# Kernel tuning notes

Hardware: AMD Instinct MI355X
Metric: run time of the kernel (lower is better)

Reference implementation:

```python
import jax, jax.numpy as jnp
import numpy as np


def setup_inputs() -> dict:
    key = jax.random.key(0)
    ks = jax.random.split(key, 32)
    B, S, H, E, Vs, T = 32, 400, 512, 300, 200, 32
    EN, V = 50000, 50200
    rn = lambda k, shape, s=0.05: jax.random.normal(k, shape, jnp.float32) * s
    return {
        'encoder_hidden': rn(ks[0], (B, S, 2 * H), 1.0),
        'hidden0': rn(ks[1], (B, H), 1.0),
        'user_embed': rn(ks[2], (B, E), 1.0),
        'W_embed': rn(ks[3], (EN, E), 1.0),
        'W_ih': rn(ks[4], (3 * H, E)), 'W_hh': rn(ks[5], (3 * H, H)),
        'b_ih': rn(ks[6], (3 * H,)), 'b_hh': rn(ks[7], (3 * H,)),
        'Wk_c': rn(ks[8], (2 * H, H)), 'bk_c': rn(ks[9], (H,)),
        'Wq_c': rn(ks[10], (H, H)), 'bq_c': rn(ks[11], (H,)),
        'we_c': rn(ks[12], (H,)), 'be_c': rn(ks[13], (1,)),
        'Wk_u': rn(ks[14], (E, H)), 'bk_u': rn(ks[15], (H,)),
        'Wq_u': rn(ks[16], (H, H)), 'bq_u': rn(ks[17], (H,)),
        'we_u': rn(ks[18], (H,)), 'be_u': rn(ks[19], (1,)),
        'Wc': rn(ks[20], (3 * H + 2 * E, H)),
        'Wg': rn(ks[21], (3 * H + E,)), 'bg': rn(ks[22], (1,)),
        'Wgen': rn(ks[23], (H, EN)),
        'src_mask': jnp.ones((B, S), jnp.int32),
        'tgt_': jax.random.randint(ks[24], (B, T), 0, EN),
        'specific_vocab': jax.random.randint(ks[25], (B, Vs), 0, EN),
        'vocab_size': V,
    }


def reference(encoder_hidden, hidden0, user_embed, W_embed, W_ih, W_hh, b_ih, b_hh,
              Wk_c, bk_c, Wq_c, bq_c, we_c, be_c, Wk_u, bk_u, Wq_u, bq_u, we_u, be_u,
              Wc, Wg, bg, Wgen, src_mask, tgt_, specific_vocab, vocab_size):
    B, T = tgt_.shape
    # teacher forcing: prev token embed, step 0 uses <s> token id 1
    tgt_embed = W_embed[tgt_]                                  # [B,T,E]
    init_embed = jnp.broadcast_to(W_embed[1], (B, 1, W_embed.shape[1]))
    prev = jnp.concatenate([init_embed, tgt_embed[:, :T - 1]], axis=1)
    xs = jnp.swapaxes(prev, 0, 1)                              # [T,B,E]

    user_vocab_emb = W_embed[specific_vocab]                   # [B,Vs,E]
    proj_key_c = encoder_hidden @ Wk_c + bk_c                  # [B,S,H]
    proj_key_u = user_vocab_emb @ Wk_u + bk_u                  # [B,Vs,H]
    mask = src_mask != 0
    batch_idx = jnp.arange(B)[:, None]

    def gru_cell(h, x):
        gi = x @ W_ih.T + b_ih
        gh = h @ W_hh.T + b_hh
        i_r, i_z, i_n = jnp.split(gi, 3, axis=-1)
        h_r, h_z, h_n = jnp.split(gh, 3, axis=-1)
        r = jax.nn.sigmoid(i_r + h_r)
        z = jax.nn.sigmoid(i_z + h_z)
        n = jnp.tanh(i_n + r * h_n)
        return (1.0 - z) * n + z * h

    def step(h, x):
        h = gru_cell(h, x)                                     # [B,H]
        q = h
        # Bahdanau attention over encoder states
        sc = jnp.tanh((q @ Wq_c + bq_c)[:, None, :] + proj_key_c) @ we_c + be_c  # [B,S]
        sc = jnp.where(mask, sc, -1e9)
        ac = jax.nn.softmax(sc, axis=-1)
        ctx_c = jnp.einsum('bs,bsd->bd', ac, encoder_hidden)   # [B,2H]
        # Bahdanau attention over user-specific vocab embeddings
        su = jnp.tanh((q @ Wq_u + bq_u)[:, None, :] + proj_key_u) @ we_u + be_u  # [B,Vs]
        au = jax.nn.softmax(su, axis=-1)
        ctx_u = jnp.einsum('bv,bve->be', au, user_vocab_emb)   # [B,E]
        ch = jnp.tanh(jnp.concatenate([q, ctx_c, ctx_u, user_embed], axis=-1) @ Wc)
        gen_prob = jax.nn.softmax(ch @ Wgen, axis=-1)          # [B,embed_num]
        gen_prob = jnp.pad(gen_prob, ((0, 0), (0, vocab_size - gen_prob.shape[-1])))
        copy_prob = jnp.zeros((B, vocab_size), gen_prob.dtype).at[batch_idx, specific_vocab].add(au)
        copy_p = jax.nn.sigmoid(jnp.concatenate([ctx_c, q, ctx_u], axis=-1) @ Wg + bg[0])[:, None]
        mix = copy_p * copy_prob + (1.0 - copy_p) * gen_prob   # [B,vocab]
        return h, mix

    _, probs = jax.lax.scan(step, hidden0, xs)                 # [T,B,V]
    return jnp.swapaxes(probs, 0, 1)                           # [B,T,V]
```

## Files before the change

### kernel.cpp

```cpp
#include <hip/hip_runtime.h>


typedef __attribute__((ext_vector_type(8))) short short8;
typedef __attribute__((ext_vector_type(4))) float f32x4;
typedef unsigned short us;

__device__ __forceinline__ float bf2f(us u) {
  return __uint_as_float(((unsigned)u) << 16);
}
__device__ __forceinline__ us f2bf(float f) {
  unsigned x = __float_as_uint(f);
  unsigned r = x + 0x7fffu + ((x >> 16) & 1u);
  return (us)(r >> 16);
}
__device__ __forceinline__ float fsigmoid(float x) { return 1.f / (1.f + __expf(-x)); }
__device__ __forceinline__ float ftanh(float x) {
  float t = __expf(-2.f * fabsf(x));
  float r = (1.f - t) / (1.f + t);
  return x >= 0.f ? r : -r;
}
__device__ __forceinline__ float ftanh_fast(float x) {
  float u = exp2f(-2.8853900817779268f * fabsf(x));
  float r = (1.f - u) * __builtin_amdgcn_rcpf(1.f + u);
  return copysignf(r, x);
}


__global__ __launch_bounds__(256) void k_cast_f2b(const float* __restrict__ src,
                                                  us* __restrict__ dst, int n4) {
  int stride = gridDim.x * blockDim.x;
  for (int i = blockIdx.x * blockDim.x + threadIdx.x; i < n4; i += stride) {
    float4 v = ((const float4*)src)[i];
    ushort4 o;
    o.x = f2bf(v.x); o.y = f2bf(v.y); o.z = f2bf(v.z); o.w = f2bf(v.w);
    ((ushort4*)dst)[i] = o;
  }
}

__global__ __launch_bounds__(256) void k_tcastX(const float* __restrict__ src0,
                                                us* __restrict__ dst0,
                                                int R, int C, int Rpad,
                                                size_t srcB, size_t dstB) {
  __shared__ float tile[32][33];
  const float* src = src0 + (size_t)blockIdx.z * srcB;
  us* dst = dst0 + (size_t)blockIdx.z * dstB;
  int c0 = blockIdx.x * 32, r0 = blockIdx.y * 32;
  int tx = threadIdx.x & 31, ty = threadIdx.x >> 5;
#pragma unroll
  for (int i = 0; i < 4; ++i) {
    int r = r0 + ty + i * 8, c = c0 + tx;
    tile[ty + i * 8][tx] = (r < R && c < C) ? src[(size_t)r * C + c] : 0.f;
  }
  __syncthreads();
#pragma unroll
  for (int i = 0; i < 4; ++i) {
    int c = c0 + ty + i * 8, rr = r0 + tx;
    if (c < C && rr < Rpad) dst[(size_t)c * Rpad + rr] = f2bf(tile[tx][ty + i * 8]);
  }
}

__global__ __launch_bounds__(256) void k_tcastXb(const us* __restrict__ src0,
                                                 us* __restrict__ dst0,
                                                 int R, int C, int Rpad,
                                                 size_t srcB, size_t dstB) {
  __shared__ us tile[32][33];
  const us* src = src0 + (size_t)blockIdx.z * srcB;
  us* dst = dst0 + (size_t)blockIdx.z * dstB;
  int c0 = blockIdx.x * 32, r0 = blockIdx.y * 32;
  int tx = threadIdx.x & 31, ty = threadIdx.x >> 5;
#pragma unroll
  for (int i = 0; i < 4; ++i) {
    int r = r0 + ty + i * 8, c = c0 + tx;
    tile[ty + i * 8][tx] = (r < R && c < C) ? src[(size_t)r * C + c] : (us)0;
  }
  __syncthreads();
#pragma unroll
  for (int i = 0; i < 4; ++i) {
    int c = c0 + ty + i * 8, rr = r0 + tx;
    if (c < C && rr < Rpad) dst[(size_t)c * Rpad + rr] = tile[tx][ty + i * 8];
  }
}

__global__ __launch_bounds__(64) void k_castpad(const float* __restrict__ src,
                                                us* __restrict__ dst,
                                                int C, int Cpad) {
  int row = blockIdx.x;
  for (int k = threadIdx.x; k < Cpad; k += 64)
    dst[(size_t)row * Cpad + k] = (k < C) ? f2bf(src[(size_t)row * C + k]) : (us)0;
}

__global__ __launch_bounds__(64) void k_gather_xe(const float* __restrict__ W_embed,
                                                  const int* __restrict__ tgt,
                                                  us* __restrict__ xe) {
  int r = blockIdx.x;
  int t = r >> 5, b = r & 31;
  int tok = (t == 0) ? 1 : tgt[b * 32 + (t - 1)];
  const float* src = W_embed + (size_t)tok * 300;
  for (int k = threadIdx.x; k < 320; k += 64)
    xe[(size_t)r * 320 + k] = (k < 300) ? f2bf(src[k]) : (us)0;
}

__global__ __launch_bounds__(64) void k_gather_uve(const float* __restrict__ W_embed,
                                                   const int* __restrict__ sv,
                                                   us* __restrict__ uve) {
  int row = blockIdx.x;
  int tok = sv[row];
  const float* src = W_embed + (size_t)tok * 300;
  for (int k = threadIdx.x; k < 320; k += 64)
    uve[(size_t)row * 320 + k] = (k < 300) ? f2bf(src[k]) : (us)0;
}

__global__ __launch_bounds__(64) void k_fragpack(const float* __restrict__ W,
                                                 us* __restrict__ F) {
  int q = blockIdx.x, lt = blockIdx.y, kt = blockIdx.z, l = threadIdx.x;
  int localrow = lt * 16 + (l & 15);
  int g = localrow >> 6, jj = localrow & 63;
  const float* src = W + (size_t)(g * 512 + q * 64 + jj) * 512 + kt * 32 + (l >> 4) * 8;
  us* dst = F + (((size_t)(q * 12 + lt) * 16 + kt) * 64 + l) * 8;
#pragma unroll
  for (int i = 0; i < 8; ++i) dst[i] = f2bf(src[i]);
}

template <int MODE>
__global__ __launch_bounds__(512) void gemm_bt(const us* __restrict__ A,
                                               const us* __restrict__ BT,
                                               int M, int N, int K, int Ntiles,
                                               const float* __restrict__ bias,
                                               us* __restrict__ outB,
                                               float* __restrict__ outF,
                                               float* __restrict__ rowsum) {
  __shared__ us As[256 * 32];
  __shared__ us Bs[128 * 32];
  __shared__ float rs[256];
  const int tid = threadIdx.x;
  const int lane = tid & 63, wid = tid >> 6;
  const int wr = wid >> 1, wc = wid & 1;
  const int bx = blockIdx.x;
  const int mt = bx / Ntiles, nt = bx - mt * Ntiles;
  const int m0 = mt * 256, n0 = nt * 128;
  f32x4 acc[4][4] = {};
  for (int kk = 0; kk < K; kk += 32) {
    uint4 av0, av1, bv;
    {
      int c = tid, row = c >> 2, c8 = (c & 3) * 8;
      av0 = *(const uint4*)(A + (size_t)(m0 + row) * K + kk + c8);
      c = tid + 512; row = c >> 2; c8 = (c & 3) * 8;
      av1 = *(const uint4*)(A + (size_t)(m0 + row) * K + kk + c8);
      c = tid; row = c >> 2; c8 = (c & 3) * 8;
      int nr = n0 + row; if (nr > N - 1) nr = N - 1;
      bv = *(const uint4*)(BT + (size_t)nr * K + kk + c8);
    }
    __syncthreads();
    ((uint4*)As)[tid] = av0;
    ((uint4*)As)[tid + 512] = av1;
    ((uint4*)Bs)[tid] = bv;
    __syncthreads();
    short8 af[4], bfr[4];
#pragma unroll
    for (int m = 0; m < 4; ++m)
      af[m] = *(const short8*)(As + (wr * 64 + m * 16 + (lane & 15)) * 32 + (lane >> 4) * 8);
#pragma unroll
    for (int n = 0; n < 4; ++n)
      bfr[n] = *(const short8*)(Bs + (wc * 64 + n * 16 + (lane & 15)) * 32 + (lane >> 4) * 8);
#pragma unroll
    for (int m = 0; m < 4; ++m)
#pragma unroll
      for (int n = 0; n < 4; ++n)
        acc[m][n] = __builtin_amdgcn_mfma_f32_16x16x32_bf16(af[m], bfr[n], acc[m][n], 0, 0, 0);
  }
  if (MODE == 0) {
#pragma unroll
    for (int m = 0; m < 4; ++m)
#pragma unroll
      for (int n = 0; n < 4; ++n)
#pragma unroll
        for (int reg = 0; reg < 4; ++reg) {
          int r = m0 + wr * 64 + m * 16 + (lane >> 4) * 4 + reg;
          int c = n0 + wc * 64 + n * 16 + (lane & 15);
          outB[(size_t)r * N + c] = f2bf(acc[m][n][reg] + bias[c]);
        }
  } else {
    if (tid < 256) rs[tid] = 0.f;
    __syncthreads();
#pragma unroll
    for (int m = 0; m < 4; ++m) {
#pragma unroll
      for (int reg = 0; reg < 4; ++reg) {
        int rloc = wr * 64 + m * 16 + (lane >> 4) * 4 + reg;
        int r = m0 + rloc;
        size_t obase = (size_t)((r & 31) * 32 + (r >> 5)) * 50200;
        float s = 0.f;
#pragma unroll
        for (int n = 0; n < 4; ++n) {
          int c = n0 + wc * 64 + n * 16 + (lane & 15);
          if (c < N) {
            float e = __expf(acc[m][n][reg]);
            if (MODE == 1) outF[obase + c] = e;
            else outB[obase + c] = f2bf(e);
            s += e;
          }
        }
        s += __shfl_xor(s, 1, 64); s += __shfl_xor(s, 2, 64);
        s += __shfl_xor(s, 4, 64); s += __shfl_xor(s, 8, 64);
        if ((lane & 15) == 0) atomicAdd(&rs[rloc], s);
      }
    }
    __syncthreads();
    if (tid < 256) atomicAdd(&rowsum[m0 + tid], rs[tid]);
  }
}

template <int MODE>
__global__ __launch_bounds__(256) void gemm_med(const us* __restrict__ A,
                                                const us* __restrict__ BT,
                                                int M, int N, int K, int Ntiles,
                                                const float* __restrict__ bias,
                                                us* __restrict__ outB) {
  __shared__ us As[64 * 32];
  __shared__ us Bs[128 * 32];
  const int tid = threadIdx.x, lane = tid & 63, w = tid >> 6;
  const int bx = blockIdx.x;
  const int mt = bx / Ntiles, nt = bx - mt * Ntiles;
  const int m0 = mt * 64, n0 = nt * 128;
  f32x4 acc[4][2] = {};
  for (int kk = 0; kk < K; kk += 32) {
    uint4 av, bv0, bv1;
    av = *(const uint4*)(A + (size_t)(m0 + (tid >> 2)) * K + kk + (tid & 3) * 8);
    {
      int i0 = tid * 2, i1 = tid * 2 + 1;
      bv0 = *(const uint4*)(BT + (size_t)(n0 + (i0 >> 2)) * K + kk + (i0 & 3) * 8);
      bv1 = *(const uint4*)(BT + (size_t)(n0 + (i1 >> 2)) * K + kk + (i1 & 3) * 8);
    }
    __syncthreads();
    ((uint4*)As)[tid] = av;
    ((uint4*)Bs)[tid * 2] = bv0;
    ((uint4*)Bs)[tid * 2 + 1] = bv1;
    __syncthreads();
    short8 af[4], bf0, bf1;
#pragma unroll
    for (int m = 0; m < 4; ++m)
      af[m] = *(const short8*)(As + (m * 16 + (lane & 15)) * 32 + (lane >> 4) * 8);
    bf0 = *(const short8*)(Bs + ((w * 2 + 0) * 16 + (lane & 15)) * 32 + (lane >> 4) * 8);
    bf1 = *(const short8*)(Bs + ((w * 2 + 1) * 16 + (lane & 15)) * 32 + (lane >> 4) * 8);
#pragma unroll
    for (int m = 0; m < 4; ++m) {
      acc[m][0] = __builtin_amdgcn_mfma_f32_16x16x32_bf16(af[m], bf0, acc[m][0], 0, 0, 0);
      acc[m][1] = __builtin_amdgcn_mfma_f32_16x16x32_bf16(af[m], bf1, acc[m][1], 0, 0, 0);
    }
  }
#pragma unroll
  for (int m = 0; m < 4; ++m)
#pragma unroll
    for (int q = 0; q < 2; ++q)
#pragma unroll
      for (int reg = 0; reg < 4; ++reg) {
        int r = m0 + m * 16 + (lane >> 4) * 4 + reg;
        int c = n0 + (w * 2 + q) * 16 + (lane & 15);
        float v = acc[m][q][reg];
        if (MODE == 0) v += bias[c];
        else v = ftanh_fast(v);
        outB[(size_t)r * N + c] = f2bf(v);
      }
}

struct FP {
  const us* frag; const us* gib; const float* bhh; const float* hidden0;
  us* hball; float* hfall; int* arrive;
  const us* encb; const us* WkcT; const float* bkc; us* pkc;
  const us* uve; const us* WkuT; const float* bku; us* pku;
  const float* Wgen; us* WT;
  const float* enc; us* encTp;
  us* uveTp;
};

__device__ void gru_body(const FP& P, int q, int tid, char* pool) {
  us* hs = (us*)pool;
  float* gh = (float*)(pool + 32768);
  const int lane = tid & 63, w = tid >> 6;
  short8 bfr[16];
  {
    const us* fb = P.frag + (((size_t)(q * 12 + w) * 16) * 64 + lane) * 8;
#pragma unroll
    for (int kt = 0; kt < 16; ++kt) bfr[kt] = *(const short8*)(fb + (size_t)kt * 512);
  }
  float hprev[3];
#pragma unroll
  for (int s = 0; s < 3; ++s) {
    int i = tid + s * 768;
    if (i < 2048) {
      int b = i >> 6, jj = i & 63;
      hprev[s] = P.hidden0[b * 512 + q * 64 + jj];
    }
  }
  const int sw = (lane & 7) << 3;
  for (int t = 0; t < 32; ++t) {
    if (t > 0) {
      if (tid == 0) {
        while (__hip_atomic_load(P.arrive + (t - 1), __ATOMIC_ACQUIRE,
                                 __HIP_MEMORY_SCOPE_AGENT) < 8) {
          __builtin_amdgcn_s_sleep(1);
        }
      }
      __syncthreads();
    }
    const us* hp = P.hball + (size_t)t * 16384;
    for (int i = tid; i < 2048; i += 768)
      ((uint4*)hs)[i ^ ((i >> 6) & 7)] = *(const uint4*)(hp + i * 8);
    __syncthreads();
    f32x4 acc0 = {}, acc1 = {};
#pragma unroll
    for (int kt = 0; kt < 16; ++kt) {
      int base0 = ((lane & 15) * 512 + kt * 32 + (lane >> 4) * 8) ^ sw;
      int base1 = (((lane & 15) + 16) * 512 + kt * 32 + (lane >> 4) * 8) ^ sw;
      short8 a0 = *(const short8*)(hs + base0);
      short8 a1 = *(const short8*)(hs + base1);
      acc0 = __builtin_amdgcn_mfma_f32_16x16x32_bf16(a0, bfr[kt], acc0, 0, 0, 0);
      acc1 = __builtin_amdgcn_mfma_f32_16x16x32_bf16(a1, bfr[kt], acc1, 0, 0, 0);
    }
    {
      int col = w * 16 + (lane & 15);
#pragma unroll
      for (int reg = 0; reg < 4; ++reg) {
        gh[col * 33 + ((lane >> 4) * 4 + reg)] = acc0[reg];
        gh[col * 33 + (16 + (lane >> 4) * 4 + reg)] = acc1[reg];
      }
    }
    __syncthreads();
    us* hbn = P.hball + (size_t)(t + 1) * 16384;
    float* hfn = P.hfall + (size_t)t * 16384;
#pragma unroll
    for (int s = 0; s < 3; ++s) {
      int i = tid + s * 768;
      if (i < 2048) {
        int b = i >> 6, jj = i & 63, j = q * 64 + jj;
        float g0 = gh[jj * 33 + b] + P.bhh[j];
        float g1 = gh[(64 + jj) * 33 + b] + P.bhh[512 + j];
        float g2 = gh[(128 + jj) * 33 + b] + P.bhh[1024 + j];
        size_t gbase = (size_t)(t * 32 + b) * 1536;
        float r_ = fsigmoid(bf2f(P.gib[gbase + j]) + g0);
        float z_ = fsigmoid(bf2f(P.gib[gbase + 512 + j]) + g1);
        float n_ = ftanh(bf2f(P.gib[gbase + 1024 + j]) + r_ * g2);
        float hv = (1.f - z_) * n_ + z_ * hprev[s];
        hprev[s] = hv;
        hbn[b * 512 + j] = f2bf(hv);
        hfn[b * 512 + j] = hv;
      }
    }
    __syncthreads();
    if (tid == 0)
      __hip_atomic_fetch_add(P.arrive + t, 1, __ATOMIC_RELEASE,
                             __HIP_MEMORY_SCOPE_AGENT);
  }
}

__device__ void gemm0_body(const us* A, const us* BT, int N, int K,
                           int mt, int nt, const float* bias, us* outB,
                           int tid, char* pool) {
  us* As = (us*)pool;
  us* Bs = (us*)(pool + 16384);
  const bool act = tid < 512;
  const int lane = tid & 63, wid = (tid >> 6) & 7;
  const int wr = wid >> 1, wc = wid & 1;
  const int m0 = mt * 256, n0 = nt * 128;
  f32x4 acc[4][4] = {};
  for (int kk = 0; kk < K; kk += 32) {
    uint4 av0 = {0, 0, 0, 0}, av1 = {0, 0, 0, 0}, bv = {0, 0, 0, 0};
    if (act) {
      int c = tid, row = c >> 2, c8 = (c & 3) * 8;
      av0 = *(const uint4*)(A + (size_t)(m0 + row) * K + kk + c8);
      av1 = *(const uint4*)(A + (size_t)(m0 + 128 + row) * K + kk + c8);
      int nr = n0 + row; if (nr > N - 1) nr = N - 1;
      bv = *(const uint4*)(BT + (size_t)nr * K + kk + c8);
    }
    __syncthreads();
    if (act) {
      ((uint4*)As)[tid] = av0;
      ((uint4*)As)[tid + 512] = av1;
      ((uint4*)Bs)[tid] = bv;
    }
    __syncthreads();
    if (act) {
      short8 af[4], bfr[4];
#pragma unroll
      for (int m = 0; m < 4; ++m)
        af[m] = *(const short8*)(As + (wr * 64 + m * 16 + (lane & 15)) * 32 + (lane >> 4) * 8);
#pragma unroll
      for (int n = 0; n < 4; ++n)
        bfr[n] = *(const short8*)(Bs + (wc * 64 + n * 16 + (lane & 15)) * 32 + (lane >> 4) * 8);
#pragma unroll
      for (int m = 0; m < 4; ++m)
#pragma unroll
        for (int n = 0; n < 4; ++n)
          acc[m][n] = __builtin_amdgcn_mfma_f32_16x16x32_bf16(af[m], bfr[n], acc[m][n], 0, 0, 0);
    }
  }
  if (act) {
#pragma unroll
    for (int m = 0; m < 4; ++m)
#pragma unroll
      for (int n = 0; n < 4; ++n)
#pragma unroll
        for (int reg = 0; reg < 4; ++reg) {
          int r = m0 + wr * 64 + m * 16 + (lane >> 4) * 4 + reg;
          int c = n0 + wc * 64 + n * 16 + (lane & 15);
          outB[(size_t)r * N + c] = f2bf(acc[m][n][reg] + bias[c]);
        }
  }
}

__global__ __launch_bounds__(768, 1) void k_fat(FP P) {
  __shared__ char pool[58368];
  const int bid = blockIdx.x, tid = threadIdx.x;
  if (bid < 8) { gru_body(P, bid, tid, pool); return; }
  if (bid < 208) {
    int j = bid - 8;
    gemm0_body(P.encb, P.WkcT, 512, 1024, j >> 2, j & 3, P.bkc, P.pkc, tid, pool);
    return;
  }
  if (bid < 308) {
    int j = bid - 208;
    gemm0_body(P.uve, P.WkuT, 512, 320, j >> 2, j & 3, P.bku, P.pku, tid, pool);
    return;
  }
  const int g = tid >> 8, lt = tid & 255;
  const int tx = lt & 31, ty = lt >> 5;
  float* tb = (float*)(pool + g * 4224);
  if (bid < 830) {
    int base = (bid - 308) * 3 + g;
    for (int it = 0; it < 16; ++it) {
      int sub = base + it * 1566;
      bool valid = sub < 25008;
      int x = valid ? sub % 1563 : 0, y = valid ? sub / 1563 : 0;
      int c0 = x * 32, r0 = y * 32;
      if (valid) {
#pragma unroll
        for (int i = 0; i < 4; ++i) {
          int r = r0 + ty + i * 8, c = c0 + tx;
          tb[(ty + i * 8) * 33 + tx] =
              (c < 50000) ? P.Wgen[(size_t)r * 50000 + c] : 0.f;
        }
      }
      __syncthreads();
      if (valid) {
#pragma unroll
        for (int i = 0; i < 4; ++i) {
          int c = c0 + ty + i * 8;
          if (c < 50000)
            P.WT[(size_t)c * 512 + r0 + tx] = f2bf(tb[tx * 33 + ty + i * 8]);
        }
      }
      __syncthreads();
    }
    return;
  }
  if (bid < 1108) {
    int base = (bid - 830) * 3 + g;
    for (int it = 0; it < 16; ++it) {
      int sub = base + it * 834;
      bool valid = sub < 13312;
      int x = sub & 31, rem = sub >> 5;
      int y = rem % 13, z = rem / 13;
      const float* src = P.enc + (size_t)z * 409600;
      us* dst = P.encTp + (size_t)z * 425984;
      int c0 = x * 32, r0 = y * 32;
      if (valid) {
#pragma unroll
        for (int i = 0; i < 4; ++i) {
          int r = r0 + ty + i * 8, c = c0 + tx;
          tb[(ty + i * 8) * 33 + tx] = (r < 400) ? src[(size_t)r * 1024 + c] : 0.f;
        }
      }
      __syncthreads();
      if (valid) {
#pragma unroll
        for (int i = 0; i < 4; ++i) {
          int c = c0 + ty + i * 8, rr = r0 + tx;
          if (rr < 416) dst[(size_t)c * 416 + rr] = f2bf(tb[tx * 33 + ty + i * 8]);
        }
      }
      __syncthreads();
    }
    return;
  }
  {
    us* tbu = (us*)tb;
    int base = (bid - 1108) * 3 + g;
    for (int it = 0; it < 16; ++it) {
      int sub = base + it * 141;
      bool valid = sub < 2240;
      int x = sub % 10, rem = sub / 10;
      int y = rem % 7, z = rem / 7;
      const us* src = P.uve + (size_t)z * 64000;
      us* dst = P.uveTp + (size_t)z * 71680;
      int c0 = x * 32, r0 = y * 32;
      if (valid) {
#pragma unroll
        for (int i = 0; i < 4; ++i) {
          int r = r0 + ty + i * 8, c = c0 + tx;
          tbu[(ty + i * 8) * 33 + tx] = (r < 200) ? src[(size_t)r * 320 + c] : (us)0;
        }
      }
      __syncthreads();
      if (valid) {
#pragma unroll
        for (int i = 0; i < 4; ++i) {
          int c = c0 + ty + i * 8, rr = r0 + tx;
          if (rr < 224) dst[(size_t)c * 224 + rr] = tbu[tx * 33 + ty + i * 8];
        }
      }
      __syncthreads();
    }
  }
}

__global__ __launch_bounds__(256) void k_scores(const us* __restrict__ Qall,
                                                const us* __restrict__ pkc,
                                                const us* __restrict__ pku,
                                                const float* __restrict__ wec,
                                                const float* __restrict__ bec,
                                                const float* __restrict__ weu,
                                                const float* __restrict__ beu,
                                                const int* __restrict__ src_mask,
                                                float* __restrict__ sc_enc,
                                                float* __restrict__ sc_usr) {
  __shared__ us q[32 * 512];
  const int bid = blockIdx.x;
  const bool enc = bid < 800;
  int b, s0, qoff, S;
  if (enc) { b = bid / 25; s0 = (bid % 25) * 16; qoff = 0; S = 400; }
  else { int j = bid - 800; b = j / 13; s0 = (j % 13) * 16; qoff = 512; S = 200; }
  for (int i = threadIdx.x; i < 2048; i += 256) {
    int tt = i >> 6, c8 = (i & 63) * 8;
    ((uint4*)q)[i] = *(const uint4*)(Qall + (size_t)(tt * 32 + b) * 1024 + qoff + c8);
  }
  const int w = threadIdx.x >> 6, lane = threadIdx.x & 63;
  const int d0 = lane * 8;
  const float* we = enc ? wec : weu;
  float wef[8];
  {
    float4 w0 = *(const float4*)(we + d0);
    float4 w1 = *(const float4*)(we + d0 + 4);
    wef[0] = w0.x; wef[1] = w0.y; wef[2] = w0.z; wef[3] = w0.w;
    wef[4] = w1.x; wef[5] = w1.y; wef[6] = w1.z; wef[7] = w1.w;
  }
  const float bias = enc ? bec[0] : beu[0];
  float pkf[4][8];
  int ss[4], validv[4], maskedv[4];
#pragma unroll
  for (int si = 0; si < 4; ++si) {
    int s = s0 + w * 4 + si;
    validv[si] = (s < S);
    int sc = validv[si] ? s : (S - 1);
    ss[si] = sc;
    const us* pk = enc ? pkc + ((size_t)b * 400 + sc) * 512
                       : pku + ((size_t)b * 200 + sc) * 512;
    uint4 pkv = *(const uint4*)(pk + d0);
    pkf[si][0] = bf2f((us)(pkv.x & 0xffff)); pkf[si][1] = bf2f((us)(pkv.x >> 16));
    pkf[si][2] = bf2f((us)(pkv.y & 0xffff)); pkf[si][3] = bf2f((us)(pkv.y >> 16));
    pkf[si][4] = bf2f((us)(pkv.z & 0xffff)); pkf[si][5] = bf2f((us)(pkv.z >> 16));
    pkf[si][6] = bf2f((us)(pkv.w & 0xffff)); pkf[si][7] = bf2f((us)(pkv.w >> 16));
    maskedv[si] = enc ? (src_mask[b * 400 + sc] == 0) : 0;
  }
  __syncthreads();
  for (int t = 0; t < 32; ++t) {
    short8 qv = *(const short8*)(q + t * 512 + d0);
    float qf[8];
#pragma unroll
    for (int d = 0; d < 8; ++d) qf[d] = bf2f((us)qv[d]);
#pragma unroll
    for (int si = 0; si < 4; ++si) {
      float a = 0.f;
#pragma unroll
      for (int d = 0; d < 8; ++d) {
        float x = qf[d] + pkf[si][d];
        float u = exp2f(-2.8853900817779268f * fabsf(x));
        float r2 = (1.f - u) * __builtin_amdgcn_rcpf(1.f + u);
        a = fmaf(copysignf(r2, x), wef[d], a);
      }
#pragma unroll
      for (int m = 1; m < 64; m <<= 1) a += __shfl_xor(a, m, 64);
      if (lane == 0 && validv[si]) {
        float v = a + bias;
        if (enc) sc_enc[(size_t)(t * 32 + b) * 400 + ss[si]] = maskedv[si] ? -1e9f : v;
        else sc_usr[(size_t)(t * 32 + b) * 200 + ss[si]] = v;
      }
    }
  }
}

__device__ __forceinline__ float bmax256(float v, float* r4, int tid) {
#pragma unroll
  for (int m = 1; m < 64; m <<= 1) v = fmaxf(v, __shfl_xor(v, m, 64));
  if ((tid & 63) == 0) r4[tid >> 6] = v;
  __syncthreads();
  float x = fmaxf(fmaxf(r4[0], r4[1]), fmaxf(r4[2], r4[3]));
  __syncthreads();
  return x;
}
__device__ __forceinline__ float bsum256(float v, float* r4, int tid) {
#pragma unroll
  for (int m = 1; m < 64; m <<= 1) v += __shfl_xor(v, m, 64);
  if ((tid & 63) == 0) r4[tid >> 6] = v;
  __syncthreads();
  float x = r4[0] + r4[1] + r4[2] + r4[3];
  __syncthreads();
  return x;
}

__global__ __launch_bounds__(256) void k_softmax(const float* __restrict__ sc_enc,
                                                 const float* __restrict__ sc_usr,
                                                 const float* __restrict__ bg,
                                                 us* __restrict__ AC,
                                                 us* __restrict__ AU,
                                                 float* __restrict__ aual,
                                                 float* __restrict__ cp_acc) {
  __shared__ float r4[4];
  int r = blockIdx.x, tid = threadIdx.x;
  if (r < 1024) {
    int t = r >> 5, b = r & 31;
    float v0 = (tid < 400) ? sc_enc[(size_t)r * 400 + tid] : -3e38f;
    float v1 = (tid + 256 < 400) ? sc_enc[(size_t)r * 400 + tid + 256] : -3e38f;
    float mx = bmax256(fmaxf(v0, v1), r4, tid);
    float e0 = (tid < 400) ? __expf(v0 - mx) : 0.f;
    float e1 = (tid + 256 < 400) ? __expf(v1 - mx) : 0.f;
    float inv = 1.f / bsum256(e0 + e1, r4, tid);
    us* ACb = AC + (size_t)(b * 32 + t) * 416;
    if (tid < 400) ACb[tid] = f2bf(e0 * inv);
    int s2 = tid + 256;
    if (s2 < 400) ACb[s2] = f2bf(e1 * inv);
    else if (s2 < 416) ACb[s2] = 0;
    if (tid == 0) cp_acc[r] = bg[0];
  } else {
    int rr = r - 1024;
    int t = rr >> 5, b = rr & 31;
    float v0 = (tid < 200) ? sc_usr[(size_t)rr * 200 + tid] : -3e38f;
    float mx = bmax256(v0, r4, tid);
    float e0 = (tid < 200) ? __expf(v0 - mx) : 0.f;
    float inv = 1.f / bsum256(e0, r4, tid);
    us* AUb = AU + (size_t)(b * 32 + t) * 224;
    if (tid < 200) {
      float a = e0 * inv;
      AUb[tid] = f2bf(a);
      aual[(size_t)rr * 200 + tid] = a;
    } else if (tid < 224) {
      AUb[tid] = 0;
    }
  }
}

__global__ __launch_bounds__(256) void k_ctx(const us* __restrict__ A,
                                             const us* __restrict__ BT,
                                             const float* __restrict__ Wg,
                                             us* __restrict__ catall,
                                             float* __restrict__ cp_acc,
                                             int N, int Kp, int catOff, int wgOff,
                                             int Nvalid) {
  __shared__ us As[32 * 32];
  __shared__ us Bs[128 * 32];
  __shared__ float gaccs[32];
  const int b = blockIdx.y, n0 = blockIdx.x * 128;
  const us* Ab = A + (size_t)b * 32 * Kp;
  const us* Bb = BT + (size_t)b * N * Kp;
  const int tid = threadIdx.x, lane = tid & 63, w = tid >> 6;
  if (tid < 32) gaccs[tid] = 0.f;
// ... 121 lines not shown
    ob[i * 2] = o0;
    ob[i * 2 + 1] = o1;
  }
  __syncthreads();
  if (t < 200) {
    int idx = sv[b * 200 + t];
    atomicAdd(out + obase + idx, cp * au_all[(size_t)r * 200 + t]);
  }
}


extern "C" void kernel_launch(void* const* d_in, const int* in_sizes, int n_in,
                              void* d_out, int out_size, void* d_ws, size_t ws_size,
                              hipStream_t stream) {
  (void)in_sizes; (void)n_in; (void)out_size;
  const float* enc = (const float*)d_in[0];
  const float* hidden0 = (const float*)d_in[1];
  const float* user_embed = (const float*)d_in[2];
  const float* W_embed = (const float*)d_in[3];
  const float* W_ih = (const float*)d_in[4];
  const float* W_hh = (const float*)d_in[5];
  const float* b_ih = (const float*)d_in[6];
  const float* b_hh = (const float*)d_in[7];
  const float* Wk_c = (const float*)d_in[8];
  const float* bk_c = (const float*)d_in[9];
  const float* Wq_c = (const float*)d_in[10];
  const float* bq_c = (const float*)d_in[11];
  const float* we_c = (const float*)d_in[12];
  const float* be_c = (const float*)d_in[13];
  const float* Wk_u = (const float*)d_in[14];
  const float* bk_u = (const float*)d_in[15];
  const float* Wq_u = (const float*)d_in[16];
  const float* bq_u = (const float*)d_in[17];
  const float* we_u = (const float*)d_in[18];
  const float* be_u = (const float*)d_in[19];
  const float* Wc = (const float*)d_in[20];
  const float* Wg = (const float*)d_in[21];
  const float* bg = (const float*)d_in[22];
  const float* Wgen = (const float*)d_in[23];
  const int* src_mask = (const int*)d_in[24];
  const int* tgt = (const int*)d_in[25];
  const int* sv = (const int*)d_in[26];
  float* out = (float*)d_out;

  char* base = (char*)d_ws;
  size_t off = 0;
  auto take = [&](size_t bytes) {
    char* p = base + off;
    off += (bytes + 255) & ~(size_t)255;
    return p;
  };
  us* WT = (us*)take(50000ull * 512 * 2);
  char* R0 = take(32ull * 1024 * 416 * 2);
  us* encb = (us*)R0;
  char* RCD = take(12800ull * 512 * 2 + 6400ull * 512 * 2);
  us* pkc = (us*)RCD;
  us* pku = (us*)(RCD + 12800ull * 512 * 2);
  us* AC = (us*)RCD;
  us* AU = (us*)(RCD + 860160);
  float* aual = (float*)(RCD + 860160 + 458752);
  us* catall = (us*)(RCD + 860160 + 458752 + 819200);
  us* chb = (us*)(RCD + 860160 + 458752 + 819200 + 4390912);
  char* RU = take(6400ull * 320 * 2);
  us* uve = (us*)RU;
  float* sc_enc = (float*)RU;
  float* sc_usr = (float*)(RU + 1024ull * 400 * 4);
  us* uveTp = (us*)take(32ull * 320 * 224 * 2);
  char* RG = take(2700000);
  us* WkcT = (us*)RG;
  us* WihT = (us*)(RG + 1048576);
  us* xe = (us*)(RG + 1048576 + 983040);
  us* Qall = (us*)RG;
  us* WkuT = (us*)take(512ull * 320 * 2);
  us* WqcuT = (us*)take(1024ull * 512 * 2);
  us* WcT = (us*)take(512ull * 2144 * 2);
  us* WhhF = (us*)take(1536ull * 512 * 2);
  us* gib = (us*)take(1024ull * 1536 * 2);
  us* hball = (us*)take(33ull * 16384 * 2);
  float* hfall = (float*)take(32ull * 16384 * 4);
  float* bqcu = (float*)take(1024 * 4);
  float* cp_acc = (float*)take(1024 * 4);
  float* cp_all = (float*)take(1024 * 4);
  float* rsum = (float*)take(1024 * 4);
  int* arrive = (int*)take(32 * 4);
  size_t expb_bytes = 1024ull * 50200 * 2;
  bool big_ws = (ws_size >= off + expb_bytes + 256);
  us* expb = big_ws ? (us*)take(expb_bytes) : nullptr;
  us* encTp = big_ws ? expb : (us*)R0;

  hipMemcpyAsync(bqcu, bq_c, 512 * 4, hipMemcpyDeviceToDevice, stream);
  hipMemcpyAsync(bqcu + 512, bq_u, 512 * 4, hipMemcpyDeviceToDevice, stream);
  hipMemsetAsync(rsum, 0, 1024 * 4, stream);
  hipMemsetAsync(arrive, 0, 32 * 4, stream);

  k_cast_f2b<<<2048, 256, 0, stream>>>(enc, encb, 3276800);
  k_cast_f2b<<<16, 256, 0, stream>>>(hidden0, hball, 4096);
  k_tcastX<<<dim3(16, 32, 1), 256, 0, stream>>>(Wk_c, WkcT, 1024, 512, 1024, 0, 0);
  k_tcastX<<<dim3(16, 10, 1), 256, 0, stream>>>(Wk_u, WkuT, 300, 512, 320, 0, 0);
  k_tcastX<<<dim3(16, 16, 1), 256, 0, stream>>>(Wq_c, WqcuT, 512, 512, 512, 0, 0);
  k_tcastX<<<dim3(16, 16, 1), 256, 0, stream>>>(Wq_u, WqcuT + 512ull * 512, 512, 512, 512, 0, 0);
  k_tcastX<<<dim3(16, 67, 1), 256, 0, stream>>>(Wc, WcT, 2136, 512, 2144, 0, 0);
  k_castpad<<<1536, 64, 0, stream>>>(W_ih, WihT, 300, 320);
  k_fragpack<<<dim3(8, 12, 16), 64, 0, stream>>>(W_hh, WhhF);
  k_gather_xe<<<1024, 64, 0, stream>>>(W_embed, tgt, xe);
  k_gather_uve<<<6400, 64, 0, stream>>>(W_embed, sv, uve);
  gemm_med<0><<<192, 256, 0, stream>>>(xe, WihT, 1024, 1536, 320, 12, b_ih, gib);

  FP fp;
  fp.frag = WhhF; fp.gib = gib; fp.bhh = b_hh; fp.hidden0 = hidden0;
  fp.hball = hball; fp.hfall = hfall; fp.arrive = arrive;
  fp.encb = encb; fp.WkcT = WkcT; fp.bkc = bk_c; fp.pkc = pkc;
  fp.uve = uve; fp.WkuT = WkuT; fp.bku = bk_u; fp.pku = pku;
  fp.Wgen = Wgen; fp.WT = WT; fp.enc = enc; fp.encTp = encTp; fp.uveTp = uveTp;

  if (big_ws) {
    k_fat<<<1155, 768, 0, stream>>>(fp);
  } else {
    k_tcastX<<<dim3(1563, 16, 1), 256, 0, stream>>>(Wgen, WT, 512, 50000, 512, 0, 0);
    gemm_bt<0><<<200, 512, 0, stream>>>(encb, WkcT, 12800, 512, 1024, 4, bk_c, pkc,
                                        nullptr, nullptr);
    gemm_bt<0><<<100, 512, 0, stream>>>(uve, WkuT, 6400, 512, 320, 4, bk_u, pku,
                                        nullptr, nullptr);
    k_tcastX<<<dim3(32, 13, 32), 256, 0, stream>>>(enc, encTp, 400, 1024, 416,
                                                   400ull * 1024, 1024ull * 416);
    k_tcastXb<<<dim3(10, 7, 32), 256, 0, stream>>>(uve, uveTp, 200, 320, 224,
                                                   200ull * 320, 320ull * 224);
    k_fat<<<8, 768, 0, stream>>>(fp);
  }

  gemm_med<0><<<128, 256, 0, stream>>>(hball + 16384, WqcuT, 1024, 1024, 512, 8,
                                       bqcu, Qall);
  k_scores<<<1216, 256, 0, stream>>>(Qall, pkc, pku, we_c, be_c, we_u, be_u,
                                     src_mask, sc_enc, sc_usr);
  k_softmax<<<2048, 256, 0, stream>>>(sc_enc, sc_usr, bg, AC, AU, aual, cp_acc);
  k_ctx<<<dim3(8, 32), 256, 0, stream>>>(AC, encTp, Wg, catall, cp_acc,
                                         1024, 416, 512, 0, 1024);
  k_ctx<<<dim3(3, 32), 256, 0, stream>>>(AU, uveTp, Wg, catall, cp_acc,
                                         320, 224, 1536, 1536, 300);
  k_catgate<<<1024, 256, 0, stream>>>(hball, hfall, user_embed, Wg, cp_acc,
                                      catall, cp_all);
  gemm_med<2><<<64, 256, 0, stream>>>(catall, WcT, 1024, 512, 2144, 4, nullptr, chb);
  if (big_ws) {
    gemm_bt<3><<<4 * 391, 512, 0, stream>>>(chb, WT, 1024, 50000, 512, 391, nullptr,
                                            expb, nullptr, rsum);
    k_finalize2<<<1024, 256, 0, stream>>>(expb, rsum, cp_all, aual, sv, out);
  } else {
    gemm_bt<1><<<4 * 391, 512, 0, stream>>>(chb, WT, 1024, 50000, 512, 391, nullptr,
                                            nullptr, out, rsum);
    k_finalize<<<1024, 256, 0, stream>>>(out, rsum, cp_all, aual, sv);
  }
}
```

Before: 735.2 us.

## Fuse prep kernels, fold tanh scale into weights, overlap input GEMM with GRU

Merges roughly a dozen small cast, transpose and gather launches into one k_prep kernel that dispatches on block index. The tanh exponent scale is folded into the key and query projection weights and biases, so the score inner loop drops a multiply. The GRU input-projection GEMM moves into k_fat, and the GRU blocks spin on an arrival counter until it finishes. Other changes: the logits epilogue now stages bf16 exp values in shared memory for 16-byte coalesced stores, and k_scores is split over time halves to double the grid. These changes cut launch overhead and ALU work but add spin-wait coupling and a larger shared-memory footprint in k_fat.

```diff
diff --git a/kernel.cpp b/kernel.cpp
--- a/kernel.cpp
+++ b/kernel.cpp
@@ -4,6 +4,8 @@
 typedef __attribute__((ext_vector_type(8))) short short8;
 typedef __attribute__((ext_vector_type(4))) float f32x4;
 typedef unsigned short us;
+
+#define SCW (-2.8853900817779268f)
 
 __device__ __forceinline__ float bf2f(us u) {
   return __uint_as_float(((unsigned)u) << 16);
@@ -20,20 +22,95 @@
   return x >= 0.f ? r : -r;
 }
 __device__ __forceinline__ float ftanh_fast(float x) {
-  float u = exp2f(-2.8853900817779268f * fabsf(x));
+  float u = exp2f(SCW * fabsf(x));
   float r = (1.f - u) * __builtin_amdgcn_rcpf(1.f + u);
   return copysignf(r, x);
 }
 
-
-__global__ __launch_bounds__(256) void k_cast_f2b(const float* __restrict__ src,
-                                                  us* __restrict__ dst, int n4) {
-  int stride = gridDim.x * blockDim.x;
-  for (int i = blockIdx.x * blockDim.x + threadIdx.x; i < n4; i += stride) {
-    float4 v = ((const float4*)src)[i];
+struct PP {
+  const float *enc, *hidden0, *Wk_c, *Wk_u, *Wq_c, *Wq_u, *Wc, *W_ih, *W_hh, *W_embed;
+  const int *tgt, *sv;
+  us *encb, *hball, *WkcT, *WkuT, *WqcuT, *WcT, *WihT, *WhhF, *xe, *uve;
+};
+
+__device__ void tcast_job(const float* __restrict__ src, us* __restrict__ dst,
+                          int R, int C, int Rpad, int x, int y, float scale,
+                          int lt, float* tb) {
+  int tx = lt & 31, ty = lt >> 5;
+  int c0 = x * 32, r0 = y * 32;
+#pragma unroll
+  for (int i = 0; i < 4; ++i) {
+    int r = r0 + ty + i * 8, c = c0 + tx;
+    tb[(ty + i * 8) * 33 + tx] = (r < R && c < C) ? src[(size_t)r * C + c] : 0.f;
+  }
+  __syncthreads();
+#pragma unroll
+  for (int i = 0; i < 4; ++i) {
+    int c = c0 + ty + i * 8, rr = r0 + tx;
+    if (c < C && rr < Rpad)
+      dst[(size_t)c * Rpad + rr] = f2bf(scale * tb[tx * 33 + ty + i * 8]);
+  }
+}
+
+__global__ __launch_bounds__(256) void k_prep(PP P) {
+  __shared__ float tb[32 * 33];
+  const int bid = blockIdx.x, tid = threadIdx.x;
+  if (bid < 1024) {
+    for (int i = bid * 256 + tid; i < 3276800; i += 1024 * 256) {
+      float4 v = ((const float4*)P.enc)[i];
+      ushort4 o;
+      o.x = f2bf(v.x); o.y = f2bf(v.y); o.z = f2bf(v.z); o.w = f2bf(v.w);
+      ((ushort4*)P.encb)[i] = o;
+    }
+  } else if (bid < 1040) {
+    int i = (bid - 1024) * 256 + tid;
+    float4 v = ((const float4*)P.hidden0)[i];
     ushort4 o;
     o.x = f2bf(v.x); o.y = f2bf(v.y); o.z = f2bf(v.z); o.w = f2bf(v.w);
-    ((ushort4*)dst)[i] = o;
+    ((ushort4*)P.hball)[i] = o;
+  } else if (bid < 1552) {
+    int j = bid - 1040;
+    tcast_job(P.Wk_c, P.WkcT, 1024, 512, 1024, j & 15, j >> 4, SCW, tid, tb);
+  } else if (bid < 1712) {
+    int j = bid - 1552;
+    tcast_job(P.Wk_u, P.WkuT, 300, 512, 320, j % 16, j / 16, SCW, tid, tb);
+  } else if (bid < 1968) {
+    int j = bid - 1712;
+    tcast_job(P.Wq_c, P.WqcuT, 512, 512, 512, j & 15, j >> 4, SCW, tid, tb);
+  } else if (bid < 2224) {
+    int j = bid - 1968;
+    tcast_job(P.Wq_u, P.WqcuT + 512ull * 512, 512, 512, 512, j & 15, j >> 4, SCW, tid, tb);
+  } else if (bid < 3296) {
+    int j = bid - 2224;
+    tcast_job(P.Wc, P.WcT, 2136, 512, 2144, j % 16, j / 16, 1.f, tid, tb);
+  } else if (bid < 3680) {
+    int row = (bid - 3296) * 4 + (tid >> 6), k = tid & 63;
+    for (int kk = k; kk < 320; kk += 64)
+      P.WihT[(size_t)row * 320 + kk] =
+          (kk < 300) ? f2bf(P.W_ih[(size_t)row * 300 + kk]) : (us)0;
+  } else if (bid < 4064) {
+    int job = (bid - 3680) * 4 + (tid >> 6), l = tid & 63;
+    int q = job / 192, rem = job - q * 192, lt2 = rem >> 4, kt = rem & 15;
+    int localrow = lt2 * 16 + (l & 15);
+    int g = localrow >> 6, jj = localrow & 63;
+    const float* src =
+        P.W_hh + (size_t)(g * 512 + q * 64 + jj) * 512 + kt * 32 + (l >> 4) * 8;
+    us* dst = P.WhhF + (((size_t)(q * 12 + lt2) * 16 + kt) * 64 + l) * 8;
+#pragma unroll
+    for (int i = 0; i < 8; ++i) dst[i] = f2bf(src[i]);
+  } else if (bid < 4320) {
+    int r = (bid - 4064) * 4 + (tid >> 6), k = tid & 63;
+    int t = r >> 5, b = r & 31;
+    int tok = (t == 0) ? 1 : P.tgt[b * 32 + (t - 1)];
+    const float* src = P.W_embed + (size_t)tok * 300;
+    for (int kk = k; kk < 320; kk += 64)
+      P.xe[(size_t)r * 320 + kk] = (kk < 300) ? f2bf(src[kk]) : (us)0;
+  } else {
+    int row = (bid - 4320) * 4 + (tid >> 6), k = tid & 63;
+    int tok = P.sv[row];
+    const float* src = P.W_embed + (size_t)tok * 300;
+    for (int kk = k; kk < 320; kk += 64)
+      P.uve[(size_t)row * 320 + kk] = (kk < 300) ? f2bf(src[kk]) : (us)0;
   }
 }
 
@@ -41,24 +118,11 @@
                                                 us* __restrict__ dst0,
                                                 int R, int C, int Rpad,
                                                 size_t srcB, size_t dstB) {
-  __shared__ float tile[32][33];
+  __shared__ float tile[32 * 33];
   const float* src = src0 + (size_t)blockIdx.z * srcB;
   us* dst = dst0 + (size_t)blockIdx.z * dstB;
-  int c0 = blockIdx.x * 32, r0 = blockIdx.y * 32;
-  int tx = threadIdx.x & 31, ty = threadIdx.x >> 5;
-#pragma unroll
-  for (int i = 0; i < 4; ++i) {
-    int r = r0 + ty + i * 8, c = c0 + tx;
-    tile[ty + i * 8][tx] = (r < R && c < C) ? src[(size_t)r * C + c] : 0.f;
-  }
-  __syncthreads();
-#pragma unroll
-  for (int i = 0; i < 4; ++i) {
-    int c = c0 + ty + i * 8, rr = r0 + tx;
-    if (c < C && rr < Rpad) dst[(size_t)c * Rpad + rr] = f2bf(tile[tx][ty + i * 8]);
-  }
-}
-
+  tcast_job(src, dst, R, C, Rpad, blockIdx.x, blockIdx.y, 1.f, threadIdx.x, tile);
+}
 __global__ __launch_bounds__(256) void k_tcastXb(const us* __restrict__ src0,
                                                  us* __restrict__ dst0,
                                                  int R, int C, int Rpad,
@@ -81,57 +145,19 @@
   }
 }
 
-__global__ __launch_bounds__(64) void k_castpad(const float* __restrict__ src,
-                                                us* __restrict__ dst,
-                                                int C, int Cpad) {
-  int row = blockIdx.x;
-  for (int k = threadIdx.x; k < Cpad; k += 64)
-    dst[(size_t)row * Cpad + k] = (k < C) ? f2bf(src[(size_t)row * C + k]) : (us)0;
-}
-
-__global__ __launch_bounds__(64) void k_gather_xe(const float* __restrict__ W_embed,
-                                                  const int* __restrict__ tgt,
-                                                  us* __restrict__ xe) {
-  int r = blockIdx.x;
-  int t = r >> 5, b = r & 31;
-  int tok = (t == 0) ? 1 : tgt[b * 32 + (t - 1)];
-  const float* src = W_embed + (size_t)tok * 300;
-  for (int k = threadIdx.x; k < 320; k += 64)
-    xe[(size_t)r * 320 + k] = (k < 300) ? f2bf(src[k]) : (us)0;
-}
-
-__global__ __launch_bounds__(64) void k_gather_uve(const float* __restrict__ W_embed,
-                                                   const int* __restrict__ sv,
-                                                   us* __restrict__ uve) {
-  int row = blockIdx.x;
-  int tok = sv[row];
-  const float* src = W_embed + (size_t)tok * 300;
-  for (int k = threadIdx.x; k < 320; k += 64)
-    uve[(size_t)row * 320 + k] = (k < 300) ? f2bf(src[k]) : (us)0;
-}
-
-__global__ __launch_bounds__(64) void k_fragpack(const float* __restrict__ W,
-                                                 us* __restrict__ F) {
-  int q = blockIdx.x, lt = blockIdx.y, kt = blockIdx.z, l = threadIdx.x;
-  int localrow = lt * 16 + (l & 15);
-  int g = localrow >> 6, jj = localrow & 63;
-  const float* src = W + (size_t)(g * 512 + q * 64 + jj) * 512 + kt * 32 + (l >> 4) * 8;
-  us* dst = F + (((size_t)(q * 12 + lt) * 16 + kt) * 64 + l) * 8;
-#pragma unroll
-  for (int i = 0; i < 8; ++i) dst[i] = f2bf(src[i]);
-}
-
 template <int MODE>
 __global__ __launch_bounds__(512) void gemm_bt(const us* __restrict__ A,
                                                const us* __restrict__ BT,
                                                int M, int N, int K, int Ntiles,
                                                const float* __restrict__ bias,
+                                               float bscale,
                                                us* __restrict__ outB,
                                                float* __restrict__ outF,
                                                float* __restrict__ rowsum) {
-  __shared__ us As[256 * 32];
-  __shared__ us Bs[128 * 32];
+  __shared__ us sh[12288];
   __shared__ float rs[256];
+  us* As = sh;
+  us* Bs = sh + 8192;
   const int tid = threadIdx.x;
   const int lane = tid & 63, wid = tid >> 6;
   const int wr = wid >> 1, wc = wid & 1;
@@ -177,7 +203,7 @@
         for (int reg = 0; reg < 4; ++reg) {
           int r = m0 + wr * 64 + m * 16 + (lane >> 4) * 4 + reg;
           int c = n0 + wc * 64 + n * 16 + (lane & 15);
-          outB[(size_t)r * N + c] = f2bf(acc[m][n][reg] + bias[c]);
+          outB[(size_t)r * N + c] = f2bf(acc[m][n][reg] + bscale * bias[c]);
         }
   } else {
     if (tid < 256) rs[tid] = 0.f;
@@ -187,22 +213,37 @@
 #pragma unroll
       for (int reg = 0; reg < 4; ++reg) {
         int rloc = wr * 64 + m * 16 + (lane >> 4) * 4 + reg;
-        int r = m0 + rloc;
-        size_t obase = (size_t)((r & 31) * 32 + (r >> 5)) * 50200;
         float s = 0.f;
 #pragma unroll
         for (int n = 0; n < 4; ++n) {
           int c = n0 + wc * 64 + n * 16 + (lane & 15);
-          if (c < N) {
-            float e = __expf(acc[m][n][reg]);
-            if (MODE == 1) outF[obase + c] = e;
-            else outB[obase + c] = f2bf(e);
-            s += e;
+          float e = (c < N) ? __expf(acc[m][n][reg]) : 0.f;
+          if (MODE == 3) {
+            int lrow = wr * 16 + (lane >> 4) * 4 + reg;
+            int lcol = wc * 64 + n * 16 + (lane & 15);
+            sh[lrow * 136 + lcol] = f2bf(e);
+          } else if (c < N) {
+            int r = m0 + rloc;
+            size_t obase = (size_t)((r & 31) * 32 + (r >> 5)) * 50200;
+            outF[obase + c] = e;
           }
+          s += e;
         }
         s += __shfl_xor(s, 1, 64); s += __shfl_xor(s, 2, 64);
         s += __shfl_xor(s, 4, 64); s += __shfl_xor(s, 8, 64);
         if ((lane & 15) == 0) atomicAdd(&rs[rloc], s);
+      }
+      if (MODE == 3) {
+        __syncthreads();
+#pragma unroll
+        for (int k2 = 0; k2 < 2; ++k2) {
+          int idx = tid + k2 * 512;
+          int l = idx >> 4, u = idx & 15;
+          int r = m0 + (l >> 4) * 64 + m * 16 + (l & 15);
+          size_t obase = (size_t)((r & 31) * 32 + (r >> 5)) * 50200;
+          *(uint4*)(outB + obase + n0 + u * 8) = *(const uint4*)(sh + l * 136 + u * 8);
+        }
+        __syncthreads();
       }
     }
     __syncthreads();
@@ -215,6 +256,7 @@
                                                 const us* __restrict__ BT,
                                                 int M, int N, int K, int Ntiles,
                                                 const float* __restrict__ bias,
+                                                float bscale,
                                                 us* __restrict__ outB) {
   __shared__ us As[64 * 32];
   __shared__ us Bs[128 * 32];
@@ -257,7 +299,7 @@
         int r = m0 + m * 16 + (lane >> 4) * 4 + reg;
         int c = n0 + (w * 2 + q) * 16 + (lane & 15);
         float v = acc[m][q][reg];
-        if (MODE == 0) v += bias[c];
+        if (MODE == 0) v += bscale * bias[c];
         else v = ftanh_fast(v);
         outB[(size_t)r * N + c] = f2bf(v);
       }
@@ -266,6 +308,7 @@
 struct FP {
   const us* frag; const us* gib; const float* bhh; const float* hidden0;
   us* hball; float* hfall; int* arrive;
+  const us* xe; const us* WihT; const float* bih; us* gibout;
   const us* encb; const us* WkcT; const float* bkc; us* pkc;
   const us* uve; const us* WkuT; const float* bku; us* pku;
   const float* Wgen; us* WT;
@@ -292,6 +335,13 @@
       hprev[s] = P.hidden0[b * 512 + q * 64 + jj];
     }
   }
+  if (tid == 0) {
+    while (__hip_atomic_load(P.arrive + 32, __ATOMIC_ACQUIRE,
+                             __HIP_MEMORY_SCOPE_AGENT) < 48) {
+      __builtin_amdgcn_s_sleep(1);
+    }
+  }
+  __syncthreads();
   const int sw = (lane & 7) << 3;
   for (int t = 0; t < 32; ++t) {
     if (t > 0) {
@@ -354,8 +404,8 @@
 }
 
 __device__ void gemm0_body(const us* A, const us* BT, int N, int K,
-                           int mt, int nt, const float* bias, us* outB,
-                           int tid, char* pool) {
+                           int mt, int nt, const float* bias, float bscale,
+                           us* outB, int tid, char* pool) {
   us* As = (us*)pool;
   us* Bs = (us*)(pool + 16384);
   const bool act = tid < 512;
@@ -403,30 +453,39 @@
         for (int reg = 0; reg < 4; ++reg) {
           int r = m0 + wr * 64 + m * 16 + (lane >> 4) * 4 + reg;
           int c = n0 + wc * 64 + n * 16 + (lane & 15);
-          outB[(size_t)r * N + c] = f2bf(acc[m][n][reg] + bias[c]);
+          outB[(size_t)r * N + c] = f2bf(acc[m][n][reg] + bscale * bias[c]);
         }
   }
 }
 
 __global__ __launch_bounds__(768, 1) void k_fat(FP P) {
-  __shared__ char pool[58368];
+  __shared__ char pool[98304];
   const int bid = blockIdx.x, tid = threadIdx.x;
   if (bid < 8) { gru_body(P, bid, tid, pool); return; }
-  if (bid < 208) {
+  if (bid < 56) {
     int j = bid - 8;
-    gemm0_body(P.encb, P.WkcT, 512, 1024, j >> 2, j & 3, P.bkc, P.pkc, tid, pool);
+    gemm0_body(P.xe, P.WihT, 1536, 320, j / 12, j % 12, P.bih, 1.f, P.gibout, tid, pool);
+    __syncthreads();
+    if (tid == 0)
+      __hip_atomic_fetch_add(P.arrive + 32, 1, __ATOMIC_RELEASE,
+                             __HIP_MEMORY_SCOPE_AGENT);
     return;
   }
-  if (bid < 308) {
-    int j = bid - 208;
-    gemm0_body(P.uve, P.WkuT, 512, 320, j >> 2, j & 3, P.bku, P.pku, tid, pool);
+  if (bid < 256) {
+    int j = bid - 56;
+    gemm0_body(P.encb, P.WkcT, 512, 1024, j >> 2, j & 3, P.bkc, SCW, P.pkc, tid, pool);
+    return;
+  }
+  if (bid < 356) {
+    int j = bid - 256;
+    gemm0_body(P.uve, P.WkuT, 512, 320, j >> 2, j & 3, P.bku, SCW, P.pku, tid, pool);
     return;
   }
   const int g = tid >> 8, lt = tid & 255;
   const int tx = lt & 31, ty = lt >> 5;
   float* tb = (float*)(pool + g * 4224);
-  if (bid < 830) {
-    int base = (bid - 308) * 3 + g;
+  if (bid < 878) {
+    int base = (bid - 356) * 3 + g;
     for (int it = 0; it < 16; ++it) {
       int sub = base + it * 1566;
       bool valid = sub < 25008;
@@ -453,8 +512,8 @@
     }
     return;
   }
-  if (bid < 1108) {
-    int base = (bid - 830) * 3 + g;
+  if (bid < 1156) {
+    int base = (bid - 878) * 3 + g;
     for (int it = 0; it < 16; ++it) {
       int sub = base + it * 834;
       bool valid = sub < 13312;
@@ -484,7 +543,7 @@
   }
   {
     us* tbu = (us*)tb;
-    int base = (bid - 1108) * 3 + g;
+    int base = (bid - 1156) * 3 + g;
     for (int it = 0; it < 16; ++it) {
       int sub = base + it * 141;
       bool valid = sub < 2240;
@@ -523,14 +582,22 @@
                                                 const int* __restrict__ src_mask,
                                                 float* __restrict__ sc_enc,
                                                 float* __restrict__ sc_usr) {
-  __shared__ us q[32 * 512];
+  __shared__ us q[16 * 512];
   const int bid = blockIdx.x;
-  const bool enc = bid < 800;
-  int b, s0, qoff, S;
-  if (enc) { b = bid / 25; s0 = (bid % 25) * 16; qoff = 0; S = 400; }
-  else { int j = bid - 800; b = j / 13; s0 = (j % 13) * 16; qoff = 512; S = 200; }
-  for (int i = threadIdx.x; i < 2048; i += 256) {
-    int tt = i >> 6, c8 = (i & 63) * 8;
+  const bool enc = bid < 1600;
+  int b, s0, th, qoff, S;
+  if (enc) {
+    b = bid / 50;
+    int r = bid % 50;
+    s0 = (r >> 1) * 16; th = r & 1; qoff = 0; S = 400;
+  } else {
+    int j = bid - 1600;
+    b = j / 26;
+    int r = j % 26;
+    s0 = (r >> 1) * 16; th = r & 1; qoff = 512; S = 200;
+  }
+  for (int i = threadIdx.x; i < 1024; i += 256) {
+    int tt = th * 16 + (i >> 6), c8 = (i & 63) * 8;
     ((uint4*)q)[i] = *(const uint4*)(Qall + (size_t)(tt * 32 + b) * 1024 + qoff + c8);
   }
   const int w = threadIdx.x >> 6, lane = threadIdx.x & 63;
@@ -562,8 +629,8 @@
     maskedv[si] = enc ? (src_mask[b * 400 + sc] == 0) : 0;
   }
   __syncthreads();
-  for (int t = 0; t < 32; ++t) {
-    short8 qv = *(const short8*)(q + t * 512 + d0);
+  for (int tl = 0; tl < 16; ++tl) {
+    short8 qv = *(const short8*)(q + tl * 512 + d0);
     float qf[8];
 #pragma unroll
     for (int d = 0; d < 8; ++d) qf[d] = bf2f((us)qv[d]);
@@ -573,13 +640,14 @@
 #pragma unroll
       for (int d = 0; d < 8; ++d) {
         float x = qf[d] + pkf[si][d];
-        float u = exp2f(-2.8853900817779268f * fabsf(x));
-        float r2 = (1.f - u) * __builtin_amdgcn_rcpf(1.f + u);
-        a = fmaf(copysignf(r2, x), wef[d], a);
+        float u = exp2f(-fabsf(x));
+        float r2v = (1.f - u) * __builtin_amdgcn_rcpf(1.f + u);
+        a = fmaf(copysignf(r2v, -x), wef[d], a);
       }
 #pragma unroll
       for (int m = 1; m < 64; m <<= 1) a += __shfl_xor(a, m, 64);
       if (lane == 0 && validv[si]) {
+        int t = th * 16 + tl;
         float v = a + bias;
         if (enc) sc_enc[(size_t)(t * 32 + b) * 400 + ss[si]] = maskedv[si] ? -1e9f : v;
         else sc_usr[(size_t)(t * 32 + b) * 200 + ss[si]] = v;
@@ -867,7 +935,7 @@
   float* cp_acc = (float*)take(1024 * 4);
   float* cp_all = (float*)take(1024 * 4);
   float* rsum = (float*)take(1024 * 4);
-  int* arrive = (int*)take(32 * 4);
+  int* arrive = (int*)take(33 * 4);
   size_t expb_bytes = 1024ull * 50200 * 2;
   bool big_ws = (ws_size >= off + expb_bytes + 256);
   us* expb = big_ws ? (us*)take(expb_bytes) : nullptr;
@@ -876,46 +944,43 @@
   hipMemcpyAsync(bqcu, bq_c, 512 * 4, hipMemcpyDeviceToDevice, stream);
   hipMemcpyAsync(bqcu + 512, bq_u, 512 * 4, hipMemcpyDeviceToDevice, stream);
   hipMemsetAsync(rsum, 0, 1024 * 4, stream);
-  hipMemsetAsync(arrive, 0, 32 * 4, stream);
-
-  k_cast_f2b<<<2048, 256, 0, stream>>>(enc, encb, 3276800);
-  k_cast_f2b<<<16, 256, 0, stream>>>(hidden0, hball, 4096);
-  k_tcastX<<<dim3(16, 32, 1), 256, 0, stream>>>(Wk_c, WkcT, 1024, 512, 1024, 0, 0);
-  k_tcastX<<<dim3(16, 10, 1), 256, 0, stream>>>(Wk_u, WkuT, 300, 512, 320, 0, 0);
-  k_tcastX<<<dim3(16, 16, 1), 256, 0, stream>>>(Wq_c, WqcuT, 512, 512, 512, 0, 0);
-  k_tcastX<<<dim3(16, 16, 1), 256, 0, stream>>>(Wq_u, WqcuT + 512ull * 512, 512, 512, 512, 0, 0);
-  k_tcastX<<<dim3(16, 67, 1), 256, 0, stream>>>(Wc, WcT, 2136, 512, 2144, 0, 0);
-  k_castpad<<<1536, 64, 0, stream>>>(W_ih, WihT, 300, 320);
-  k_fragpack<<<dim3(8, 12, 16), 64, 0, stream>>>(W_hh, WhhF);
-  k_gather_xe<<<1024, 64, 0, stream>>>(W_embed, tgt, xe);
-  k_gather_uve<<<6400, 64, 0, stream>>>(W_embed, sv, uve);
-  gemm_med<0><<<192, 256, 0, stream>>>(xe, WihT, 1024, 1536, 320, 12, b_ih, gib);
+  hipMemsetAsync(arrive, 0, 33 * 4, stream);
+
+  PP pp;
+  pp.enc = enc; pp.hidden0 = hidden0; pp.Wk_c = Wk_c; pp.Wk_u = Wk_u;
+  pp.Wq_c = Wq_c; pp.Wq_u = Wq_u; pp.Wc = Wc; pp.W_ih = W_ih; pp.W_hh = W_hh;
+  pp.W_embed = W_embed; pp.tgt = tgt; pp.sv = sv;
+  pp.encb = encb; pp.hball = hball; pp.WkcT = WkcT; pp.WkuT = WkuT;
+  pp.WqcuT = WqcuT; pp.WcT = WcT; pp.WihT = WihT; pp.WhhF = WhhF;
+  pp.xe = xe; pp.uve = uve;
+  k_prep<<<5920, 256, 0, stream>>>(pp);
 
   FP fp;
   fp.frag = WhhF; fp.gib = gib; fp.bhh = b_hh; fp.hidden0 = hidden0;
   fp.hball = hball; fp.hfall = hfall; fp.arrive = arrive;
+  fp.xe = xe; fp.WihT = WihT; fp.bih = b_ih; fp.gibout = gib;
   fp.encb = encb; fp.WkcT = WkcT; fp.bkc = bk_c; fp.pkc = pkc;
   fp.uve = uve; fp.WkuT = WkuT; fp.bku = bk_u; fp.pku = pku;
   fp.Wgen = Wgen; fp.WT = WT; fp.enc = enc; fp.encTp = encTp; fp.uveTp = uveTp;
 
   if (big_ws) {
-    k_fat<<<1155, 768, 0, stream>>>(fp);
+    k_fat<<<1203, 768, 0, stream>>>(fp);
   } else {
     k_tcastX<<<dim3(1563, 16, 1), 256, 0, stream>>>(Wgen, WT, 512, 50000, 512, 0, 0);
-    gemm_bt<0><<<200, 512, 0, stream>>>(encb, WkcT, 12800, 512, 1024, 4, bk_c, pkc,
-                                        nullptr, nullptr);
-    gemm_bt<0><<<100, 512, 0, stream>>>(uve, WkuT, 6400, 512, 320, 4, bk_u, pku,
-                                        nullptr, nullptr);
+    gemm_bt<0><<<200, 512, 0, stream>>>(encb, WkcT, 12800, 512, 1024, 4, bk_c, SCW,
+                                        pkc, nullptr, nullptr);
+    gemm_bt<0><<<100, 512, 0, stream>>>(uve, WkuT, 6400, 512, 320, 4, bk_u, SCW,
+                                        pku, nullptr, nullptr);
     k_tcastX<<<dim3(32, 13, 32), 256, 0, stream>>>(enc, encTp, 400, 1024, 416,
                                                    400ull * 1024, 1024ull * 416);
     k_tcastXb<<<dim3(10, 7, 32), 256, 0, stream>>>(uve, uveTp, 200, 320, 224,
                                                    200ull * 320, 320ull * 224);
-    k_fat<<<8, 768, 0, stream>>>(fp);
+    k_fat<<<56, 768, 0, stream>>>(fp);
   }
 
   gemm_med<0><<<128, 256, 0, stream>>>(hball + 16384, WqcuT, 1024, 1024, 512, 8,
-                                       bqcu, Qall);
-  k_scores<<<1216, 256, 0, stream>>>(Qall, pkc, pku, we_c, be_c, we_u, be_u,
+                                       bqcu, SCW, Qall);
+  k_scores<<<2432, 256, 0, stream>>>(Qall, pkc, pku, we_c, be_c, we_u, be_u,
                                      src_mask, sc_enc, sc_usr);
   k_softmax<<<2048, 256, 0, stream>>>(sc_enc, sc_usr, bg, AC, AU, aual, cp_acc);
   k_ctx<<<dim3(8, 32), 256, 0, stream>>>(AC, encTp, Wg, catall, cp_acc,
@@ -924,14 +989,15 @@
                                          320, 224, 1536, 1536, 300);
   k_catgate<<<1024, 256, 0, stream>>>(hball, hfall, user_embed, Wg, cp_acc,
                                       catall, cp_all);
-  gemm_med<2><<<64, 256, 0, stream>>>(catall, WcT, 1024, 512, 2144, 4, nullptr, chb);
+  gemm_med<2><<<64, 256, 0, stream>>>(catall, WcT, 1024, 512, 2144, 4, nullptr,
+                                      1.f, chb);
   if (big_ws) {
     gemm_bt<3><<<4 * 391, 512, 0, stream>>>(chb, WT, 1024, 50000, 512, 391, nullptr,
-                                            expb, nullptr, rsum);
+                                            1.f, expb, nullptr, rsum);
     k_finalize2<<<1024, 256, 0, stream>>>(expb, rsum, cp_all, aual, sv, out);
   } else {
     gemm_bt<1><<<4 * 391, 512, 0, stream>>>(chb, WT, 1024, 50000, 512, 391, nullptr,
-                                            nullptr, out, rsum);
+                                            1.f, nullptr, out, rsum);
     k_finalize<<<1024, 256, 0, stream>>>(out, rsum, cp_all, aual, sv);
   }
 }
```

Result: faster. 689.5 us (-6.2%).
